# Optimization experiments

Hardware: AMD Instinct MI355X
Metric: run time of the kernel (lower is better)

The kernel has to match this reference:

```python
import jax, jax.numpy as jnp
import numpy as np

NUM_USERS = 100000
NUM_ITEMS = 50000
N_NODES = NUM_USERS + NUM_ITEMS
EMBED_DIM = 64
RECON_DIM = 32
N_LAYERS = 3
NNZ = 4800000


def setup_inputs() -> dict:
    key = jax.random.key(0)
    ks = jax.random.split(key, 8)
    adj_rows = jax.random.randint(ks[0], (NNZ,), 0, N_NODES, dtype=jnp.int32)
    adj_cols = jax.random.randint(ks[1], (NNZ,), 0, N_NODES, dtype=jnp.int32)
    # symmetric-normalized adjacency values are small positives
    adj_vals = jax.random.uniform(ks[2], (NNZ,), dtype=jnp.float32) * 0.05
    user_embeddings = jax.random.normal(ks[3], (NUM_USERS, EMBED_DIM), dtype=jnp.float32) * 0.1
    item_embeddings = jax.random.normal(ks[4], (NUM_ITEMS, EMBED_DIM), dtype=jnp.float32) * 0.1
    fc1_w = jax.random.normal(ks[5], (RECON_DIM, EMBED_DIM), dtype=jnp.float32) / np.sqrt(EMBED_DIM)
    fc1_b = jnp.zeros((RECON_DIM,), dtype=jnp.float32)
    fc2_w = jax.random.normal(ks[6], (EMBED_DIM, RECON_DIM), dtype=jnp.float32) / np.sqrt(RECON_DIM)
    fc2_b = jnp.zeros((EMBED_DIM,), dtype=jnp.float32)
    return {
        'adj_rows': adj_rows, 'adj_cols': adj_cols, 'adj_vals': adj_vals,
        'user_embeddings': user_embeddings, 'item_embeddings': item_embeddings,
        'fc1_w': fc1_w, 'fc1_b': fc1_b, 'fc2_w': fc2_w, 'fc2_b': fc2_b,
    }


def _spmm(rows, cols, vals, x, n):
    # sparse (n,n) COO @ dense (n,d)
    return jax.ops.segment_sum(vals[:, None] * x[cols], rows, num_segments=n)


def reference(adj_rows, adj_cols, adj_vals, user_embeddings, item_embeddings,
              fc1_w, fc1_b, fc2_w, fc2_b):
    n = user_embeddings.shape[0] + item_embeddings.shape[0]
    ego = jnp.concatenate([user_embeddings, item_embeddings], axis=0)  # [N, d]
    acc = ego  # running sum over layers (equivalent to stack+mean)
    for _ in range(N_LAYERS):
        ego = _spmm(adj_rows, adj_cols, adj_vals, ego, n)
        acc = acc + ego
    all_emb = acc / jnp.asarray(N_LAYERS + 1, dtype=acc.dtype)
    u = all_emb[:user_embeddings.shape[0]]
    i = all_emb[user_embeddings.shape[0]:]
    # autoencoder: encode (fc1) then decode (fc2); no activation in original
    u_gen = (u @ fc1_w.T + fc1_b) @ fc2_w.T + fc2_b
    i_gen = (i @ fc1_w.T + fc1_b) @ fc2_w.T + fc2_b
    loss = jnp.sum((u_gen - u) ** 2) + jnp.sum((i_gen - i) ** 2)
    return (u_gen, i_gen, loss)
```

## Files before the change

kernel.cpp:

```cpp
#include <hip/hip_runtime.h>

#define N_USERS 100000
#define N_ITEMS 50000
#define N_NODES 150000
#define DIM 64
#define RDIM 32
#define NNZ_E 4800000
#define EMB_TOT (N_NODES * DIM)
#define RPB 512
#define NB ((N_NODES + RPB - 1) / RPB)
#define BPART 256
#define TPART 1024

__device__ __forceinline__ unsigned short f2bf(float f) {
    unsigned u = __float_as_uint(f);
    u += 0x7FFFu + ((u >> 16) & 1u);
    return (unsigned short)(u >> 16);
}
__device__ __forceinline__ float bf2f(unsigned short b) {
    return __uint_as_float(((unsigned)b) << 16);
}

__global__ __launch_bounds__(256) void k_init16(const float4* __restrict__ ue,
                                                const float4* __restrict__ ie,
                                                ushort4* __restrict__ ego) {
    int i = blockIdx.x * 256 + threadIdx.x;
    if (i >= EMB_TOT / 4) return;
    const int USER4 = N_USERS * DIM / 4;
    float4 v = (i < USER4) ? ue[i] : ie[i - USER4];
    ushort4 o;
    o.x = f2bf(v.x); o.y = f2bf(v.y); o.z = f2bf(v.z); o.w = f2bf(v.w);
    ego[i] = o;
}

__global__ __launch_bounds__(TPART) void k_hist(const int* __restrict__ rows,
                                                int* __restrict__ hist) {
    __shared__ int h[NB];
    for (int i = threadIdx.x; i < NB; i += TPART) h[i] = 0;
    __syncthreads();
    for (int e = blockIdx.x * TPART + threadIdx.x; e < NNZ_E; e += BPART * TPART)
        atomicAdd(&h[rows[e] >> 9], 1);
    __syncthreads();
    for (int i = threadIdx.x; i < NB; i += TPART)
        hist[blockIdx.x * NB + i] = h[i];
}

__global__ __launch_bounds__(256) void k_btot(const int* __restrict__ hist,
                                              int* __restrict__ btot) {
    int b = blockIdx.x * 256 + threadIdx.x;
    if (b >= NB) return;
    int s = 0;
    for (int blk = 0; blk < BPART; ++blk) s += hist[blk * NB + b];
    btot[b] = s;
}

__global__ __launch_bounds__(1024) void k_bsum(const int* __restrict__ btot,
                                               int* __restrict__ base,
                                               int* __restrict__ rs) {
    __shared__ int sc[1024];
    int t = threadIdx.x;
    sc[t] = (t < NB) ? btot[t] : 0;
    __syncthreads();
    for (int off = 1; off < 1024; off <<= 1) {
        int v = (t >= off) ? sc[t - off] : 0;
        __syncthreads();
        sc[t] += v;
        __syncthreads();
    }
    if (t < NB) base[t] = (t == 0) ? 0 : sc[t - 1];
    if (t == 0) { base[NB] = NNZ_E; rs[N_NODES] = NNZ_E; }
}

__global__ __launch_bounds__(256) void k_off(int* __restrict__ hist,
                                             const int* __restrict__ base) {
    int b = blockIdx.x * 256 + threadIdx.x;
    if (b >= NB) return;
    int run = base[b];
    for (int blk = 0; blk < BPART; ++blk) {
        int c = hist[blk * NB + b];
        hist[blk * NB + b] = run;
        run += c;
    }
}

__global__ __launch_bounds__(TPART) void k_part(const int* __restrict__ rows,
                                                const int* __restrict__ cols,
                                                const float* __restrict__ vals,
                                                const int* __restrict__ hist,
                                                uint2* __restrict__ tmp) {
    __shared__ int cur[NB];
    for (int i = threadIdx.x; i < NB; i += TPART)
        cur[i] = hist[blockIdx.x * NB + i];
    __syncthreads();
    for (int e = blockIdx.x * TPART + threadIdx.x; e < NNZ_E; e += BPART * TPART) {
        int r = rows[e];
        int b = r >> 9;
        int pos = atomicAdd(&cur[b], 1);
        tmp[pos] = make_uint2(((unsigned)(r & 511) << 18) | (unsigned)cols[e],
                              __float_as_uint(vals[e]));
    }
}

__global__ __launch_bounds__(512) void k_sortbkt(const uint2* __restrict__ tmp,
                                                 const int* __restrict__ base,
                                                 uint2* __restrict__ edges,
                                                 int* __restrict__ rs) {
    int b = blockIdx.x;
    int gbase = base[b];
    int nE = base[b + 1] - gbase;
    int nrows = N_NODES - b * RPB;
    if (nrows > RPB) nrows = RPB;

    __shared__ int cnt[RPB];
    __shared__ int sc[RPB];
    int t = threadIdx.x;
    cnt[t] = 0;
    __syncthreads();
    for (int i = t; i < nE; i += 512)
        atomicAdd(&cnt[tmp[gbase + i].x >> 18], 1);
    __syncthreads();
    sc[t] = cnt[t];
    __syncthreads();
    for (int off = 1; off < RPB; off <<= 1) {
        int v = (t >= off) ? sc[t - off] : 0;
        __syncthreads();
        sc[t] += v;
        __syncthreads();
    }
    {
        int excl = (t == 0) ? 0 : sc[t - 1];
        if (t < nrows) rs[b * RPB + t] = gbase + excl;
        cnt[t] = excl;
    }
    __syncthreads();
    for (int i = t; i < nE; i += 512) {
        uint2 u = tmp[gbase + i];
        int rl = u.x >> 18;
        int p = atomicAdd(&cnt[rl], 1);
        edges[gbase + p] = make_uint2(u.x & 0x3FFFFu, u.y);
    }
}

__global__ __launch_bounds__(256) void k_spmm16(const uint2* __restrict__ edges,
                                                const int* __restrict__ rs,
                                                const unsigned short* __restrict__ x16,
                                                unsigned short* __restrict__ y16) {
    int wid  = (blockIdx.x * 256 + threadIdx.x) >> 6;
    int lane = threadIdx.x & 63;
    if (wid >= N_NODES) return;
    int start = __builtin_amdgcn_readfirstlane(rs[wid]);
    int end   = __builtin_amdgcn_readfirstlane(rs[wid + 1]);
    const unsigned short* xl = x16 + lane;
    float s = 0.0f;
    #pragma unroll 8
    for (int j = start; j < end; ++j) {
        uint2 e = edges[j];
        s += __uint_as_float(e.y) * bf2f(xl[(int)e.x << 6]);
    }
    y16[(wid << 6) + lane] = f2bf(s);
}

__global__ void k_zero_loss(float* p) {
    if (blockIdx.x == 0 && threadIdx.x == 0) *p = 0.0f;
}

__global__ __launch_bounds__(256) void k_mlp_loss(const float* __restrict__ ue,
                                                  const float* __restrict__ ie,
                                                  const unsigned short* __restrict__ s1,
                                                  const unsigned short* __restrict__ s2,
                                                  const unsigned short* __restrict__ s3,
                                                  float* __restrict__ out,
                                                  const float* __restrict__ w1,
                                                  const float* __restrict__ b1,
                                                  const float* __restrict__ w2,
                                                  const float* __restrict__ b2,
                                                  float* __restrict__ loss) {
    __shared__ float sw1[RDIM][DIM];
    __shared__ float sw2[DIM][RDIM];
    __shared__ float sb1[RDIM];
    __shared__ float sb2[DIM];

    for (int i = threadIdx.x; i < RDIM * DIM; i += 256) sw1[i / DIM][i % DIM] = w1[i];
    for (int i = threadIdx.x; i < DIM * RDIM; i += 256) sw2[i / RDIM][i % RDIM] = w2[i];
    if (threadIdx.x < RDIM) sb1[threadIdx.x] = b1[threadIdx.x];
    if (threadIdx.x < DIM)  sb2[threadIdx.x] = b2[threadIdx.x];
    __syncthreads();

    int r = blockIdx.x * 256 + threadIdx.x;
    float lsum = 0.0f;
    if (r < N_NODES) {
        const float* ego = (r < N_USERS) ? (ue + (size_t)r * DIM)
                                         : (ie + (size_t)(r - N_USERS) * DIM);
        float e[DIM];
        {
            const float4*  e4 = (const float4*)ego;
            const ushort4* p1 = (const ushort4*)(s1 + ((size_t)r << 6));
            const ushort4* p2 = (const ushort4*)(s2 + ((size_t)r << 6));
            const ushort4* p3 = (const ushort4*)(s3 + ((size_t)r << 6));
            #pragma unroll
            for (int q = 0; q < DIM / 4; ++q) {
                float4 v = e4[q];
                ushort4 a = p1[q], b = p2[q], c = p3[q];
                e[4 * q + 0] = 0.25f * (v.x + bf2f(a.x) + bf2f(b.x) + bf2f(c.x));
                e[4 * q + 1] = 0.25f * (v.y + bf2f(a.y) + bf2f(b.y) + bf2f(c.y));
                e[4 * q + 2] = 0.25f * (v.z + bf2f(a.z) + bf2f(b.z) + bf2f(c.z));
                e[4 * q + 3] = 0.25f * (v.w + bf2f(a.w) + bf2f(b.w) + bf2f(c.w));
            }
        }
        float h[RDIM];
        #pragma unroll
        for (int j = 0; j < RDIM; ++j) {
            float s = sb1[j];
            #pragma unroll
            for (int d = 0; d < DIM; ++d) s += sw1[j][d] * e[d];
            h[j] = s;
        }
        float4* rowp = (float4*)(out + ((size_t)r << 6));
        #pragma unroll
        for (int q = 0; q < DIM / 4; ++q) {
            float g[4];
            #pragma unroll
            for (int m = 0; m < 4; ++m) {
                int k = 4 * q + m;
                float s = sb2[k];
                #pragma unroll
                for (int j = 0; j < RDIM; ++j) s += sw2[k][j] * h[j];
                g[m] = s;
                float df = s - e[k];
                lsum += df * df;
            }
            float4 v;
            v.x = g[0]; v.y = g[1]; v.z = g[2]; v.w = g[3];
            rowp[q] = v;
        }
    }

    #pragma unroll
    for (int off = 32; off > 0; off >>= 1) lsum += __shfl_down(lsum, off);
    __shared__ float wsum[4];
    if ((threadIdx.x & 63) == 0) wsum[threadIdx.x >> 6] = lsum;
    __syncthreads();
    if (threadIdx.x == 0) {
        atomicAdd(loss, wsum[0] + wsum[1] + wsum[2] + wsum[3]);
    }
}

extern "C" void kernel_launch(void* const* d_in, const int* in_sizes, int n_in,
                              void* d_out, int out_size, void* d_ws, size_t ws_size,
                              hipStream_t stream) {
    const int*   rows = (const int*)d_in[0];
    const int*   cols = (const int*)d_in[1];
    const float* vals = (const float*)d_in[2];
    const float* ue   = (const float*)d_in[3];
    const float* ie   = (const float*)d_in[4];
    const float* w1   = (const float*)d_in[5];
    const float* b1   = (const float*)d_in[6];
    const float* w2   = (const float*)d_in[7];
    const float* b2   = (const float*)d_in[8];
    float* out = (float*)d_out;

    unsigned short* regA = (unsigned short*)d_ws;
    unsigned short* regB = regA + 2 * EMB_TOT;
    uint2* tmp   = (uint2*)regB;
    uint2* edges = (uint2*)(regB + 2 * EMB_TOT);
    int*   hist  = (int*)(edges + NNZ_E);
    int*   btot  = hist + BPART * NB;
    int*   base  = btot + NB;
    int*   rs    = base + NB + 1;

    unsigned short* ego0 = regB;
    unsigned short* s1   = regB + EMB_TOT;
    unsigned short* s2   = regA;
    unsigned short* s3   = regA + EMB_TOT;

    const int VEC_BLOCKS  = (EMB_TOT / 4 + 255) / 256;
    const int SPMM_BLOCKS = (N_NODES * 64 + 255) / 256;

    k_hist<<<BPART, TPART, 0, stream>>>(rows, hist);
    k_btot<<<(NB + 255) / 256, 256, 0, stream>>>(hist, btot);
    k_bsum<<<1, 1024, 0, stream>>>(btot, base, rs);
    k_off<<<(NB + 255) / 256, 256, 0, stream>>>(hist, base);
    k_part<<<BPART, TPART, 0, stream>>>(rows, cols, vals, hist, tmp);
    k_sortbkt<<<NB, 512, 0, stream>>>(tmp, base, edges, rs);

    k_init16<<<VEC_BLOCKS, 256, 0, stream>>>((const float4*)ue, (const float4*)ie,
                                             (ushort4*)ego0);

    k_spmm16<<<SPMM_BLOCKS, 256, 0, stream>>>(edges, rs, ego0, s1);
    k_spmm16<<<SPMM_BLOCKS, 256, 0, stream>>>(edges, rs, s1, s2);
    k_spmm16<<<SPMM_BLOCKS, 256, 0, stream>>>(edges, rs, s2, s3);

    k_zero_loss<<<1, 64, 0, stream>>>(out + EMB_TOT);
    k_mlp_loss<<<(N_NODES + 255) / 256, 256, 0, stream>>>(ue, ie, s1, s2, s3,
                                                          out, w1, b1, w2, b2,
                                                          out + EMB_TOT);
}
```

Measured before the change: 683.5 us.

## Split each MLP row across four threads with shuffle-reduced hidden layer

The fused MLP/loss kernel now assigns four threads per node row, each handling a 16-wide slice of the embedding. Partial fc1 dot products are combined with xor shuffles across the four lanes, and each thread then computes and writes its own 16 outputs. The aim is to cut per-thread register pressure (no 64-float array), raise occupancy, and make the row loads more coalesced. The cost is four times as many blocks, redundant fc1 bias adds and shuffle work, and the previous single-thread-per-row design is gone.

```diff
diff --git a/kernel.cpp b/kernel.cpp
--- a/kernel.cpp
+++ b/kernel.cpp
@@ -186,47 +186,66 @@
     if (threadIdx.x < DIM)  sb2[threadIdx.x] = b2[threadIdx.x];
     __syncthreads();
 
-    int r = blockIdx.x * 256 + threadIdx.x;
-    float lsum = 0.0f;
-    if (r < N_NODES) {
+    int t = threadIdx.x;
+    int r = blockIdx.x * 64 + (t >> 2);
+    int p = t & 3;
+    bool valid = (r < N_NODES);
+
+    float e[16];
+    float h[RDIM];
+    #pragma unroll
+    for (int j = 0; j < RDIM; ++j) h[j] = 0.0f;
+
+    if (valid) {
         const float* ego = (r < N_USERS) ? (ue + (size_t)r * DIM)
                                          : (ie + (size_t)(r - N_USERS) * DIM);
-        float e[DIM];
-        {
-            const float4*  e4 = (const float4*)ego;
-            const ushort4* p1 = (const ushort4*)(s1 + ((size_t)r << 6));
-            const ushort4* p2 = (const ushort4*)(s2 + ((size_t)r << 6));
-            const ushort4* p3 = (const ushort4*)(s3 + ((size_t)r << 6));
-            #pragma unroll
-            for (int q = 0; q < DIM / 4; ++q) {
-                float4 v = e4[q];
-                ushort4 a = p1[q], b = p2[q], c = p3[q];
-                e[4 * q + 0] = 0.25f * (v.x + bf2f(a.x) + bf2f(b.x) + bf2f(c.x));
-                e[4 * q + 1] = 0.25f * (v.y + bf2f(a.y) + bf2f(b.y) + bf2f(c.y));
-                e[4 * q + 2] = 0.25f * (v.z + bf2f(a.z) + bf2f(b.z) + bf2f(c.z));
-                e[4 * q + 3] = 0.25f * (v.w + bf2f(a.w) + bf2f(b.w) + bf2f(c.w));
-            }
+        const float4*  e4 = (const float4*)(ego + p * 16);
+        const ushort4* p1 = (const ushort4*)(s1 + ((size_t)r << 6) + p * 16);
+        const ushort4* p2 = (const ushort4*)(s2 + ((size_t)r << 6) + p * 16);
+        const ushort4* p3 = (const ushort4*)(s3 + ((size_t)r << 6) + p * 16);
+        #pragma unroll
+        for (int q = 0; q < 4; ++q) {
+            float4 v = e4[q];
+            ushort4 a = p1[q], b = p2[q], c = p3[q];
+            e[4 * q + 0] = 0.25f * (v.x + bf2f(a.x) + bf2f(b.x) + bf2f(c.x));
+            e[4 * q + 1] = 0.25f * (v.y + bf2f(a.y) + bf2f(b.y) + bf2f(c.y));
+            e[4 * q + 2] = 0.25f * (v.z + bf2f(a.z) + bf2f(b.z) + bf2f(c.z));
+            e[4 * q + 3] = 0.25f * (v.w + bf2f(a.w) + bf2f(b.w) + bf2f(c.w));
         }
-        float h[RDIM];
         #pragma unroll
         for (int j = 0; j < RDIM; ++j) {
-            float s = sb1[j];
+            float s = 0.0f;
             #pragma unroll
-            for (int d = 0; d < DIM; ++d) s += sw1[j][d] * e[d];
+            for (int d = 0; d < 16; ++d) s += sw1[j][p * 16 + d] * e[d];
             h[j] = s;
         }
-        float4* rowp = (float4*)(out + ((size_t)r << 6));
+    } else {
         #pragma unroll
-        for (int q = 0; q < DIM / 4; ++q) {
+        for (int d = 0; d < 16; ++d) e[d] = 0.0f;
+    }
+
+    #pragma unroll
+    for (int j = 0; j < RDIM; ++j) {
+        float v = h[j];
+        v += __shfl_xor(v, 1);
+        v += __shfl_xor(v, 2);
+        h[j] = v + sb1[j];
+    }
+
+    float lsum = 0.0f;
+    if (valid) {
+        float4* rowp = (float4*)(out + ((size_t)r << 6) + p * 16);
+        #pragma unroll
+        for (int q = 0; q < 4; ++q) {
             float g[4];
             #pragma unroll
             for (int m = 0; m < 4; ++m) {
-                int k = 4 * q + m;
+                int k = p * 16 + 4 * q + m;
                 float s = sb2[k];
                 #pragma unroll
                 for (int j = 0; j < RDIM; ++j) s += sw2[k][j] * h[j];
                 g[m] = s;
-                float df = s - e[k];
+                float df = s - e[4 * q + m];
                 lsum += df * df;
             }
             float4 v;
@@ -275,6 +294,7 @@
 
     const int VEC_BLOCKS  = (EMB_TOT / 4 + 255) / 256;
     const int SPMM_BLOCKS = (N_NODES * 64 + 255) / 256;
+    const int MLP_BLOCKS  = (N_NODES + 63) / 64;
 
     k_hist<<<BPART, TPART, 0, stream>>>(rows, hist);
     k_btot<<<(NB + 255) / 256, 256, 0, stream>>>(hist, btot);
@@ -291,7 +311,7 @@
     k_spmm16<<<SPMM_BLOCKS, 256, 0, stream>>>(edges, rs, s2, s3);
 
     k_zero_loss<<<1, 64, 0, stream>>>(out + EMB_TOT);
-    k_mlp_loss<<<(N_NODES + 255) / 256, 256, 0, stream>>>(ue, ie, s1, s2, s3,
-                                                          out, w1, b1, w2, b2,
-                                                          out + EMB_TOT);
-}
+    k_mlp_loss<<<MLP_BLOCKS, 256, 0, stream>>>(ue, ie, s1, s2, s3,
+                                               out, w1, b1, w2, b2,
+                                               out + EMB_TOT);
+}
```

After: 695.6 us. About the same (+1.8%).
